# Kernel tuning notes

Measured on AMD Instinct MI355X. Metric: run time of the kernel, lower is better.

## Reference

```python
import jax, jax.numpy as jnp
import numpy as np

B, C, H, W = 4, 96, 64, 64
NLAYERS, DSTATE, EXPAND, DCONV = 2, 16, 2, 4
DIN = EXPAND * C          # 192
DTRANK = (C + 15) // 16   # 6
EPS = 1e-5


def setup_inputs() -> dict:
    key = jax.random.key(0)
    ks = jax.random.split(key, 10)
    s = jnp.float32(0.02)
    f32 = jnp.float32
    inp = {
        "x": jax.random.normal(ks[0], (B, C, H, W), f32),
        "ln_g": jnp.ones((NLAYERS, C), f32),
        "ln_b": jnp.zeros((NLAYERS, C), f32),
        "in_w": jax.random.normal(ks[1], (NLAYERS, C, 2 * DIN), f32) * s,
        "conv_w": jax.random.normal(ks[2], (NLAYERS, DIN, DCONV), f32) * s,
        "conv_b": jnp.zeros((NLAYERS, DIN), f32),
        "xproj_w": jax.random.normal(ks[3], (NLAYERS, DIN, DTRANK + 2 * DSTATE), f32) * s,
        "dt_w": jax.random.normal(ks[4], (NLAYERS, DTRANK, DIN), f32) * s,
        "dt_b": jnp.full((NLAYERS, DIN), -4.6, f32),  # softplus(-4.6) ~ 0.01
        "A_log": jnp.log(jnp.tile(jnp.arange(1, DSTATE + 1, dtype=f32)[None, None, :], (NLAYERS, DIN, 1))),
        "Dp": jnp.ones((NLAYERS, DIN), f32),
        "out_w": jax.random.normal(ks[5], (NLAYERS, DIN, C), f32) * s,
        "gp_w": jax.random.normal(ks[6], (C, C), f32) * s,
        "gp_b": jnp.zeros((C,), f32),
        "fus_w": jax.random.normal(ks[7], (C, 2 * C), f32) * s,
        "fus_b": jnp.zeros((C,), f32),
        "bn_g": jnp.ones((C,), f32),
        "bn_b": jnp.zeros((C,), f32),
    }
    return inp


def _mamba_block(seq, ln_g, ln_b, in_w, conv_w, conv_b, xproj_w, dt_w, dt_b, A_log, Dp, out_w):
    # seq: (B, L, C)
    L = seq.shape[1]
    mu = seq.mean(-1, keepdims=True)
    var = ((seq - mu) ** 2).mean(-1, keepdims=True)
    h = (seq - mu) * jax.lax.rsqrt(var + EPS) * ln_g + ln_b
    xz = h @ in_w                                   # (B, L, 2*DIN)
    xs, z = jnp.split(xz, 2, axis=-1)
    # causal depthwise conv1d along L (kernel DCONV)
    xp = jnp.pad(xs, ((0, 0), (DCONV - 1, 0), (0, 0)))
    xc = sum(conv_w[:, k] * xp[:, k:k + L, :] for k in range(DCONV)) + conv_b
    xc = jax.nn.silu(xc)
    dbl = xc @ xproj_w                              # (B, L, DTRANK+2*DSTATE)
    dt = dbl[..., :DTRANK]
    Bm = dbl[..., DTRANK:DTRANK + DSTATE]
    Cm = dbl[..., DTRANK + DSTATE:]
    delta = jax.nn.softplus(dt @ dt_w + dt_b)       # (B, L, DIN)
    A = -jnp.exp(A_log)                             # (DIN, DSTATE)
    dA = jnp.exp(delta[..., None] * A)              # (B, L, DIN, DSTATE)
    dBx = delta[..., None] * Bm[:, :, None, :] * xc[..., None]
    def comb(a, b):  # compose linear recurrences h -> A*h + u
        return (a[0] * b[0], b[0] * a[1] + b[1])
    hstates = jax.lax.associative_scan(comb, (dA, dBx), axis=1)[1]
    y = jnp.einsum('blds,bls->bld', hstates, Cm) + Dp * xc
    y = y * jax.nn.silu(z)
    return y @ out_w


def _forward(x, ln_g, ln_b, in_w, conv_w, conv_b, xproj_w, dt_w, dt_b, A_log, Dp, out_w,
             gp_w, gp_b, fus_w, fus_b, bn_g, bn_b):
    b, c, h, w = x.shape
    L = h * w
    residual = x
    seq = x.reshape(b, c, L).transpose(0, 2, 1)     # (B, L, C)
    for i in range(NLAYERS):
        seq = seq + _mamba_block(seq, ln_g[i], ln_b[i], in_w[i], conv_w[i], conv_b[i],
                                 xproj_w[i], dt_w[i], dt_b[i], A_log[i], Dp[i], out_w[i])
    mamba_out = seq.transpose(0, 2, 1).reshape(b, c, h, w)
    # global pool -> 1x1 conv -> relu -> bilinear upsample of 1x1 == broadcast
    gp = jax.nn.relu(x.mean((2, 3)) @ gp_w.T + gp_b)          # (B, C)
    gfull = jnp.broadcast_to(gp[:, :, None, None], (b, c, h, w))
    cat = jnp.concatenate([mamba_out, gfull], axis=1)         # (B, 2C, H, W)
    out = jnp.einsum('oc,bchw->bohw', fus_w, cat) + fus_b[None, :, None, None]
    # BatchNorm2d (training-mode batch statistics)
    mu = out.mean((0, 2, 3))
    var = out.var((0, 2, 3))
    out = (out - mu[None, :, None, None]) * jax.lax.rsqrt(var + EPS)[None, :, None, None]
    out = out * bn_g[None, :, None, None] + bn_b[None, :, None, None]
    return out + residual


def reference(x, ln_g, ln_b, in_w, conv_w, conv_b, xproj_w, dt_w, dt_b, A_log, Dp, out_w,
              gp_w, gp_b, fus_w, fus_b, bn_g, bn_b):
    return _forward(x, ln_g, ln_b, in_w, conv_w, conv_b, xproj_w, dt_w, dt_b, A_log, Dp, out_w,
                    gp_w, gp_b, fus_w, fus_b, bn_g, bn_b)
```

## Files before the change

### kernel.cpp

```cpp
#include <hip/hip_runtime.h>
#include <math.h>

#define BB 4
#define C 96
#define LL 4096
#define DIN 192
#define DS 16
#define DT 6
#define DX 38
#define NCHAIN (BB*DIN*DS)
#define NBLK_FUSE 512
#define EPSF 1e-5f

__device__ __forceinline__ float silu_f(float x){ return x / (1.0f + __expf(-x)); }
__device__ __forceinline__ float softplus_f(float x){ return x > 20.0f ? x : log1pf(__expf(x)); }

__global__ void k_transpose_in(const float* __restrict__ x, float* __restrict__ seq){
    __shared__ float t[32][33];
    int b = blockIdx.z;
    int l0 = blockIdx.x*32, c0 = blockIdx.y*32;
    int tx = threadIdx.x, ty = threadIdx.y;
    t[ty][tx] = x[((size_t)b*C + c0 + ty)*LL + l0 + tx];
    __syncthreads();
    seq[((size_t)b*LL + l0 + ty)*C + c0 + tx] = t[tx][ty];
}

__global__ void k_xmean(const float* __restrict__ x, float* __restrict__ xmean){
    __shared__ float red[256];
    int bc = blockIdx.x;
    const float* p = x + (size_t)bc*LL;
    float s = 0.f;
    for (int i = threadIdx.x; i < LL; i += 256) s += p[i];
    red[threadIdx.x] = s; __syncthreads();
    for (int o = 128; o; o >>= 1){
        if (threadIdx.x < o) red[threadIdx.x] += red[threadIdx.x+o];
        __syncthreads();
    }
    if (threadIdx.x == 0) xmean[bc] = red[0] * (1.f/LL);
}

__global__ void k_prep_fusw(const float* __restrict__ fus_w, float* __restrict__ fus_wt){
    int idx = blockIdx.x*256 + threadIdx.x;
    if (idx < C*C){
        int c = idx / C, o = idx % C;
        fus_wt[idx] = fus_w[(size_t)o*(2*C) + c];
    }
}

#define XSB_OFF 0
#define HB_OFF  6720
#define XCB_OFF 6720
#define DBL_OFF 0
#define FRONT_LDS 12896

__global__ __launch_bounds__(512) void k_front(const float* __restrict__ seq,
        const float* __restrict__ ln_g, const float* __restrict__ ln_b,
        const float* __restrict__ in_w,
        const float* __restrict__ conv_w, const float* __restrict__ conv_b,
        const float* __restrict__ xproj_w, const float* __restrict__ dt_w,
        const float* __restrict__ dt_b,
        float* __restrict__ zbuf, float* __restrict__ xc,
        float* __restrict__ delta, float* __restrict__ Bm, float* __restrict__ Cm){
    __shared__ float buf[FRONT_LDS];
    float* xsb = buf + XSB_OFF;
    float* hb  = buf + HB_OFF;
    float* xcb = buf + XCB_OFF;
    float* dbl = buf + DBL_OFF;
    int tid = threadIdx.x;
    int wave = tid >> 6, lane = tid & 63;
    int bid = blockIdx.x;
    int role = bid >> 9;
    int t0 = (bid & 511)*32;
    int l0 = t0 & (LL - 1);

    if (role == 1){
        for (int r = wave; r < 32; r += 8){
            const float* row = seq + (size_t)(t0 + r)*C;
            float v0 = row[lane];
            float v1 = (lane < 32) ? row[64 + lane] : 0.f;
            float sum = v0 + v1;
            for (int off = 32; off; off >>= 1) sum += __shfl_xor(sum, off);
            float mu = sum * (1.f/C);
            float d0 = v0 - mu;
            float d1 = (lane < 32) ? (v1 - mu) : 0.f;
            float sq = d0*d0 + d1*d1;
            for (int off = 32; off; off >>= 1) sq += __shfl_xor(sq, off);
            float rstd = rsqrtf(sq * (1.f/C) + EPSF);
            hb[r*C + lane] = d0*rstd*ln_g[lane] + ln_b[lane];
            if (lane < 32) hb[r*C + 64 + lane] = d1*rstd*ln_g[64+lane] + ln_b[64+lane];
        }
        __syncthreads();
        float acc[4][3];
        #pragma unroll
        for (int k = 0; k < 4; k++)
            #pragma unroll
            for (int j = 0; j < 3; j++) acc[k][j] = 0.f;
        int tw = wave*4;
        for (int c = 0; c < C; c++){
            const float* wr = in_w + (size_t)c*(2*DIN) + DIN;
            float w0 = wr[lane], w1 = wr[lane+64], w2 = wr[lane+128];
            #pragma unroll
            for (int k = 0; k < 4; k++){
                float hv = hb[(tw + k)*C + c];
                acc[k][0] = fmaf(hv, w0, acc[k][0]);
                acc[k][1] = fmaf(hv, w1, acc[k][1]);
                acc[k][2] = fmaf(hv, w2, acc[k][2]);
            }
        }
        #pragma unroll
        for (int k = 0; k < 4; k++){
            float* zp = zbuf + (size_t)(t0 + tw + k)*DIN;
            zp[lane]       = acc[k][0];
            zp[64 + lane]  = acc[k][1];
            zp[128 + lane] = acc[k][2];
        }
        return;
    }

    for (int r = wave; r < 35; r += 8){
        bool valid = (l0 > 0) || (r >= 3);
        float h0 = 0.f, h1 = 0.f;
        if (valid){
            const float* row = seq + (size_t)(t0 - 3 + r)*C;
            float v0 = row[lane];
            float v1 = (lane < 32) ? row[64 + lane] : 0.f;
            float sum = v0 + v1;
            for (int off = 32; off; off >>= 1) sum += __shfl_xor(sum, off);
            float mu = sum * (1.f/C);
            float d0 = v0 - mu;
            float d1 = (lane < 32) ? (v1 - mu) : 0.f;
            float sq = d0*d0 + d1*d1;
            for (int off = 32; off; off >>= 1) sq += __shfl_xor(sq, off);
            float rstd = rsqrtf(sq * (1.f/C) + EPSF);
            h0 = d0*rstd*ln_g[lane] + ln_b[lane];
            if (lane < 32) h1 = d1*rstd*ln_g[64+lane] + ln_b[64+lane];
        }
        hb[r*C + lane] = h0;
        if (lane < 32) hb[r*C + 64 + lane] = h1;
    }
    __syncthreads();
    int rows[5];
    #pragma unroll
    for (int k = 0; k < 5; k++){
        int r = wave + 8*k;
        rows[k] = (r < 35) ? r : 34;
    }
    float acc[5][3];
    #pragma unroll
    for (int k = 0; k < 5; k++)
        #pragma unroll
        for (int j = 0; j < 3; j++) acc[k][j] = 0.f;
    for (int c = 0; c < C; c++){
        const float* wr = in_w + (size_t)c*(2*DIN);
        float w0 = wr[lane], w1 = wr[lane+64], w2 = wr[lane+128];
        #pragma unroll
        for (int k = 0; k < 5; k++){
            float hv = hb[rows[k]*C + c];
            acc[k][0] = fmaf(hv, w0, acc[k][0]);
            acc[k][1] = fmaf(hv, w1, acc[k][1]);
            acc[k][2] = fmaf(hv, w2, acc[k][2]);
        }
    }
    #pragma unroll
    for (int k = 0; k < 5; k++){
        int r = wave + 8*k;
        if (r < 35){
            xsb[r*DIN + lane]       = acc[k][0];
            xsb[r*DIN + 64 + lane]  = acc[k][1];
            xsb[r*DIN + 128 + lane] = acc[k][2];
        }
    }
    __syncthreads();
    for (int idx = tid; idx < 32*DIN; idx += 512){
        int tl = idx / DIN, d = idx % DIN;
        const float* cw = conv_w + d*4;
        float a = conv_b[d];
        a = fmaf(cw[0], xsb[(tl+0)*DIN + d], a);
        a = fmaf(cw[1], xsb[(tl+1)*DIN + d], a);
        a = fmaf(cw[2], xsb[(tl+2)*DIN + d], a);
        a = fmaf(cw[3], xsb[(tl+3)*DIN + d], a);
        float s = silu_f(a);
        xcb[tl*(DIN+1) + d] = s;
        xc[(size_t)(t0 + tl)*DIN + d] = s;
    }
    __syncthreads();
    for (int idx = tid; idx < 32*DX; idx += 512){
        int tl = idx / DX, o = idx % DX;
        const float* wo = xproj_w + o;
        float a0 = 0.f, a1 = 0.f;
        for (int c = 0; c < DIN; c += 2){
            a0 = fmaf(xcb[tl*(DIN+1) + c],   wo[(size_t)c*DX],     a0);
            a1 = fmaf(xcb[tl*(DIN+1) + c+1], wo[(size_t)(c+1)*DX], a1);
        }
        float a = a0 + a1;
        dbl[tl*DX + o] = a;
        int tg = t0 + tl;
        if (o >= DT && o < DT+DS)      Bm[(size_t)tg*DS + (o-DT)] = a;
        else if (o >= DT+DS)           Cm[(size_t)tg*DS + (o-DT-DS)] = a;
    }
    __syncthreads();
    for (int idx = tid; idx < 32*DIN; idx += 512){
        int tl = idx / DIN, d = idx % DIN;
        float a = dt_b[d];
        #pragma unroll
        for (int r = 0; r < DT; r++) a = fmaf(dbl[tl*DX + r], dt_w[r*DIN + d], a);
        delta[(size_t)(t0 + tl)*DIN + d] = softplus_f(a);
    }
}

template<int NCHT>
__global__ __launch_bounds__(384) void k_scan_A(const float* __restrict__ delta,
        const float* __restrict__ xc, const float* __restrict__ Bm,
        const float* __restrict__ A_log,
        float* __restrict__ Pbuf, float* __restrict__ Sbuf){
    const int CLT = LL / NCHT;
    int tid = threadIdx.x;
    int d = tid >> 1, half = tid & 1;
    int ch = blockIdx.x % NCHT;
    int b  = blockIdx.x / NCHT;
    const float4* ap = (const float4*)(A_log + (size_t)d*DS + half*8);
    float4 a0 = ap[0], a1 = ap[1];
    float Av[8] = {a0.x,a0.y,a0.z,a0.w, a1.x,a1.y,a1.z,a1.w};
    float P[8], hs[8];
    #pragma unroll
    for (int s = 0; s < 8; s++){ Av[s] = -__expf(Av[s]); P[s] = 1.f; hs[s] = 0.f; }
    size_t tbase = (size_t)b*LL + (size_t)ch*CLT;
    const float*  dp = delta + tbase*DIN + d;
    const float*  xp = xc    + tbase*DIN + d;
    const float4* bp = (const float4*)(Bm + tbase*DS + half*8);
    for (int i = 0; i < CLT; i++){
        float dv = dp[(size_t)i*DIN];
        float xv = xp[(size_t)i*DIN];
        float4 b0 = bp[4*i], b1 = bp[4*i+1];
        float bb[8] = {b0.x,b0.y,b0.z,b0.w, b1.x,b1.y,b1.z,b1.w};
        float dxv = dv*xv;
        #pragma unroll
        for (int s = 0; s < 8; s++){
            float dA = __expf(dv*Av[s]);
            hs[s] = fmaf(dA, hs[s], bb[s]*dxv);
            P[s] *= dA;
        }
    }
    size_t base = (size_t)ch*NCHAIN + ((size_t)b*DIN + d)*DS + half*8;
    float4* Pb = (float4*)(Pbuf + base);
    float4* Sb = (float4*)(Sbuf + base);
    Pb[0] = make_float4(P[0],P[1],P[2],P[3]);
    Pb[1] = make_float4(P[4],P[5],P[6],P[7]);
    Sb[0] = make_float4(hs[0],hs[1],hs[2],hs[3]);
    Sb[1] = make_float4(hs[4],hs[5],hs[6],hs[7]);
}

template<int NCHT>
__global__ void k_scan_B(const float* __restrict__ Pbuf, float* __restrict__ Sbuf){
    int chain = blockIdx.x*256 + threadIdx.x;
    float h = 0.f;
    for (int ch = 0; ch < NCHT; ch++){
        size_t idx = (size_t)ch*NCHAIN + chain;
        float P = Pbuf[idx];
        float S = Sbuf[idx];
        Sbuf[idx] = h;
        h = fmaf(P, h, S);
    }
}

template<int NCHT>
__global__ __launch_bounds__(384) void k_scan_C(const float* __restrict__ delta,
        const float* __restrict__ xc, const float* __restrict__ Bm,
        const float* __restrict__ Cm,
        const float* __restrict__ A_log, const float* __restrict__ Dp,
        const float* __restrict__ Sbuf, float* __restrict__ yraw){
    const int CLT = LL / NCHT;
    int tid = threadIdx.x;
    int d = tid >> 1, half = tid & 1;
    int ch = blockIdx.x % NCHT;
    int b  = blockIdx.x / NCHT;
    const float4* ap = (const float4*)(A_log + (size_t)d*DS + half*8);
    float4 a0 = ap[0], a1 = ap[1];
    float Av[8] = {a0.x,a0.y,a0.z,a0.w, a1.x,a1.y,a1.z,a1.w};
    #pragma unroll
    for (int s = 0; s < 8; s++) Av[s] = -__expf(Av[s]);
    float Dv = Dp[d];
    size_t base = (size_t)ch*NCHAIN + ((size_t)b*DIN + d)*DS + half*8;
    const float4* Sb = (const float4*)(Sbuf + base);
    float4 h0 = Sb[0], h1 = Sb[1];
    float h[8] = {h0.x,h0.y,h0.z,h0.w, h1.x,h1.y,h1.z,h1.w};
    size_t tbase = (size_t)b*LL + (size_t)ch*CLT;
    const float*  dp = delta + tbase*DIN + d;
    const float*  xp = xc    + tbase*DIN + d;
    const float4* bp = (const float4*)(Bm + tbase*DS + half*8);
    const float4* cp = (const float4*)(Cm + tbase*DS + half*8);
    float* yp = yraw + tbase*DIN + d;
    for (int i = 0; i < CLT; i++){
        float dv = dp[(size_t)i*DIN];
        float xv = xp[(size_t)i*DIN];
        float4 b0 = bp[4*i], b1 = bp[4*i+1];
        float4 c0 = cp[4*i], c1 = cp[4*i+1];
        float bb[8] = {b0.x,b0.y,b0.z,b0.w, b1.x,b1.y,b1.z,b1.w};
        float cc[8] = {c0.x,c0.y,c0.z,c0.w, c1.x,c1.y,c1.z,c1.w};
        float dxv = dv*xv;
        float acc0 = 0.f, acc1 = 0.f;
        #pragma unroll
        for (int s = 0; s < 8; s += 2){
            float dA0 = __expf(dv*Av[s]);
            float dA1 = __expf(dv*Av[s+1]);
            h[s]   = fmaf(dA0, h[s],   bb[s]*dxv);
            h[s+1] = fmaf(dA1, h[s+1], bb[s+1]*dxv);
            acc0 = fmaf(h[s],   cc[s],   acc0);
            acc1 = fmaf(h[s+1], cc[s+1], acc1);
        }
        float contrib = acc0 + acc1;
        if (half == 0) contrib += Dv*xv;
        contrib += __shfl_xor(contrib, 1);
        if (half == 0) yp[(size_t)i*DIN] = contrib;
    }
}

__global__ __launch_bounds__(512) void k_outproj(const float* __restrict__ yraw,
        const float* __restrict__ zbuf, const float* __restrict__ out_w,
        float* __restrict__ seq){
    __shared__ float ygb[32][DIN];
    int tid = threadIdx.x;
    int wave = tid >> 6, lane = tid & 63;
    int t0 = blockIdx.x*32;
    for (int idx = tid; idx < 32*DIN; idx += 512){
        int tl = idx / DIN, d = idx % DIN;
        int t = t0 + tl;
        float yv = yraw[(size_t)t*DIN + d];
        float zv = zbuf[(size_t)t*DIN + d];
        ygb[tl][d] = yv * silu_f(zv);
    }
    __syncthreads();
    float a0[4], a1[4];
    #pragma unroll
    for (int t = 0; t < 4; t++){ a0[t] = 0.f; a1[t] = 0.f; }
    int tw = wave*4;
    for (int d = 0; d < DIN; d++){
        const float* wr = out_w + (size_t)d*C;
        float w0 = wr[lane];
        float w1 = (lane < 32) ? wr[64 + lane] : 0.f;
        #pragma unroll
        for (int t = 0; t < 4; t++){
            float yv = ygb[tw + t][d];
            a0[t] = fmaf(yv, w0, a0[t]);
            a1[t] = fmaf(yv, w1, a1[t]);
        }
    }
    #pragma unroll
    for (int t = 0; t < 4; t++){
        size_t tg = (size_t)(t0 + tw + t);
        seq[tg*C + lane] += a0[t];
        if (lane < 32) seq[tg*C + 64 + lane] += a1[t];
    }
}

__global__ void k_gp(const float* __restrict__ xmean, const float* __restrict__ gp_w,
        const float* __restrict__ gp_b, const float* __restrict__ fus_w,
        const float* __restrict__ fus_b, float* __restrict__ gconst){
    __shared__ float gp[BB*C];
    int tid = threadIdx.x;
    int b = tid / C, i = tid % C;
    float a = gp_b[i];
    for (int c = 0; c < C; c++) a = fmaf(xmean[b*C + c], gp_w[i*C + c], a);
    gp[tid] = fmaxf(a, 0.f);
    __syncthreads();
    float g = fus_b[i];
    for (int c = 0; c < C; c++) g = fmaf(fus_w[i*(2*C) + C + c], gp[b*C + c], g);
    gconst[tid] = g;
}

__global__ __launch_bounds__(512) void k_fuse(const float* __restrict__ seq,
        const float* __restrict__ fus_wt, const float* __restrict__ gconst,
        float* __restrict__ outpre, float* __restrict__ psum, float* __restrict__ psq){
    __shared__ float sb[32][C];
    __shared__ float bs[8][C], bq[8][C];
    int tid = threadIdx.x;
    int wave = tid >> 6, lane = tid & 63;
    int t0 = blockIdx.x*32;
    int b = t0 >> 12;
    for (int idx = tid; idx < 32*C; idx += 512){
        int tl = idx / C, c = idx % C;
        sb[tl][c] = seq[(size_t)(t0 + tl)*C + c];
    }
    __syncthreads();
    float g0 = gconst[b*C + lane];
    float g1 = (lane < 32) ? gconst[b*C + 64 + lane] : 0.f;
    float a0[4], a1[4];
    #pragma unroll
    for (int t = 0; t < 4; t++){ a0[t] = g0; a1[t] = g1; }
    int tw = wave*4;
    for (int c = 0; c < C; c++){
        const float* wr = fus_wt + (size_t)c*C;
        float w0 = wr[lane];
        float w1 = (lane < 32) ? wr[64 + lane] : 0.f;
        #pragma unroll
        for (int t = 0; t < 4; t++){
            float sv = sb[tw + t][c];
            a0[t] = fmaf(sv, w0, a0[t]);
            a1[t] = fmaf(sv, w1, a1[t]);
        }
    }
    float s0 = 0.f, q0 = 0.f, s1 = 0.f, q1 = 0.f;
    #pragma unroll
    for (int t = 0; t < 4; t++){
        size_t tg = (size_t)(t0 + tw + t);
        outpre[tg*C + lane] = a0[t];
        s0 += a0[t]; q0 += a0[t]*a0[t];
        if (lane < 32){
            outpre[tg*C + 64 + lane] = a1[t];
            s1 += a1[t]; q1 += a1[t]*a1[t];
        }
    }
    bs[wave][lane] = s0; bq[wave][lane] = q0;
    if (lane < 32){ bs[wave][64+lane] = s1; bq[wave][64+lane] = q1; }
    __syncthreads();
    if (tid < C){
        float s = 0.f, q = 0.f;
        #pragma unroll
        for (int w = 0; w < 8; w++){ s += bs[w][tid]; q += bq[w][tid]; }
        psum[(size_t)blockIdx.x*C + tid] = s;
        psq [(size_t)blockIdx.x*C + tid] = q;
    }
}

__global__ void k_bnstat(const float* __restrict__ psum, const float* __restrict__ psq,
        const float* __restrict__ bn_g, const float* __restrict__ bn_b,
        float* __restrict__ scale, float* __restrict__ shift){
    __shared__ float r1[256], r2[256];
    int o = blockIdx.x;
    float s1 = 0.f, s2 = 0.f;
    for (int i = threadIdx.x; i < NBLK_FUSE; i += 256){
        s1 += psum[(size_t)i*C + o];
        s2 += psq [(size_t)i*C + o];
    }
    r1[threadIdx.x] = s1; r2[threadIdx.x] = s2; __syncthreads();
    for (int off = 128; off; off >>= 1){
        if (threadIdx.x < off){ r1[threadIdx.x] += r1[threadIdx.x+off]; r2[threadIdx.x] += r2[threadIdx.x+off]; }
        __syncthreads();
    }
    if (threadIdx.x == 0){
        float N = (float)(BB*LL);
        float mu = r1[0] / N;
        float var = r2[0] / N - mu*mu;
        float sc = bn_g[o] * rsqrtf(var + EPSF);
        scale[o] = sc;
        shift[o] = bn_b[o] - mu*sc;
    }
}

__global__ void k_final(const float* __restrict__ outpre, const float* __restrict__ x,
        const float* __restrict__ scale, const float* __restrict__ shift,
        float* __restrict__ out){
    __shared__ float tle[32][33];
    int b = blockIdx.z;
    int l0 = blockIdx.x*32, o0 = blockIdx.y*32;
    int tx = threadIdx.x, ty = threadIdx.y;
    tle[ty][tx] = outpre[((size_t)b*LL + l0 + ty)*C + o0 + tx];
    __syncthreads();
    int o = o0 + ty;
    size_t idx = ((size_t)b*C + o)*LL + l0 + tx;
    out[idx] = tle[tx][ty]*scale[o] + shift[o] + x[idx];
}

extern "C" void kernel_launch(void* const* d_in, const int* in_sizes, int n_in,
                              void* d_out, int out_size, void* d_ws, size_t ws_size,
                              hipStream_t stream){
    const float* x      = (const float*)d_in[0];
    const float* ln_g   = (const float*)d_in[1];
    const float* ln_b   = (const float*)d_in[2];
    const float* in_w   = (const float*)d_in[3];
    const float* conv_w = (const float*)d_in[4];
    const float* conv_b = (const float*)d_in[5];
    const float* xproj_w= (const float*)d_in[6];
    const float* dt_w   = (const float*)d_in[7];
    const float* dt_b   = (const float*)d_in[8];
    const float* A_log  = (const float*)d_in[9];
    const float* Dp     = (const float*)d_in[10];
    const float* out_w  = (const float*)d_in[11];
    const float* gp_w   = (const float*)d_in[12];
    const float* gp_b   = (const float*)d_in[13];
    const float* fus_w  = (const float*)d_in[14];
    const float* fus_b  = (const float*)d_in[15];
    const float* bn_g   = (const float*)d_in[16];
    const float* bn_b   = (const float*)d_in[17];

    const size_t base_f = (size_t)BB*LL*C
                        + (size_t)BB*LL*DIN
                        + (size_t)BB*LL*DIN
                        + (size_t)BB*LL*DIN
                        + (size_t)BB*LL*DS + (size_t)BB*LL*DS;
    const size_t small_f = BB*C + BB*C + C + C + (size_t)C*C;
    const size_t need256 = (base_f + 2*(size_t)256*NCHAIN + small_f) * sizeof(float);
    const int nch = (ws_size >= need256) ? 256 : 128;

    float* ws    = (float*)d_ws;
    float* seq   = ws;
    float* zbuf  = seq   + (size_t)BB*LL*C;
    float* xcbuf = zbuf  + (size_t)BB*LL*DIN;
    float* delta = xcbuf + (size_t)BB*LL*DIN;
    float* Bmb   = delta + (size_t)BB*LL*DIN;
    float* Cmb   = Bmb   + (size_t)BB*LL*DS;
    float* Pbuf  = Cmb   + (size_t)BB*LL*DS;
    float* Sbuf  = Pbuf  + (size_t)nch*NCHAIN;
    float* xmean = Sbuf  + (size_t)nch*NCHAIN;
    float* gconst= xmean + BB*C;
    float* scale = gconst+ BB*C;
    float* shift = scale + C;
    float* fus_wt= shift + C;
    float* yraw  = delta;
    float* outpre= zbuf;
    float* psum  = zbuf + (size_t)BB*LL*C;
    float* psq   = psum + (size_t)NBLK_FUSE*C;

    k_transpose_in<<<dim3(LL/32, C/32, BB), dim3(32,32), 0, stream>>>(x, seq);
    k_xmean<<<BB*C, 256, 0, stream>>>(x, xmean);
    k_prep_fusw<<<(C*C + 255)/256, 256, 0, stream>>>(fus_w, fus_wt);

    for (int layer = 0; layer < 2; layer++){
        const float* lng = ln_g   + (size_t)layer*C;
        const float* lnb = ln_b   + (size_t)layer*C;
        const float* inw = in_w   + (size_t)layer*C*2*DIN;
        const float* cw  = conv_w + (size_t)layer*DIN*4;
        const float* cb  = conv_b + (size_t)layer*DIN;
        const float* xpw = xproj_w+ (size_t)layer*DIN*DX;
        const float* dtw = dt_w   + (size_t)layer*DT*DIN;
        const float* dtb = dt_b   + (size_t)layer*DIN;
        const float* alog= A_log  + (size_t)layer*DIN*DS;
        const float* dpp = Dp     + (size_t)layer*DIN;
        const float* ow  = out_w  + (size_t)layer*DIN*C;

        k_front<<<2*(BB*LL)/32, 512, 0, stream>>>(seq, lng, lnb, inw, cw, cb,
                                                  xpw, dtw, dtb, zbuf, xcbuf, delta, Bmb, Cmb);
        if (nch == 256){
            k_scan_A<256><<<BB*256, 384, 0, stream>>>(delta, xcbuf, Bmb, alog, Pbuf, Sbuf);
            k_scan_B<256><<<NCHAIN/256, 256, 0, stream>>>(Pbuf, Sbuf);
            k_scan_C<256><<<BB*256, 384, 0, stream>>>(delta, xcbuf, Bmb, Cmb, alog, dpp, Sbuf, yraw);
        } else {
            k_scan_A<128><<<BB*128, 384, 0, stream>>>(delta, xcbuf, Bmb, alog, Pbuf, Sbuf);
            k_scan_B<128><<<NCHAIN/256, 256, 0, stream>>>(Pbuf, Sbuf);
            k_scan_C<128><<<BB*128, 384, 0, stream>>>(delta, xcbuf, Bmb, Cmb, alog, dpp, Sbuf, yraw);
        }
        k_outproj<<<(BB*LL)/32, 512, 0, stream>>>(yraw, zbuf, ow, seq);
    }

    k_gp<<<1, BB*C, 0, stream>>>(xmean, gp_w, gp_b, fus_w, fus_b, gconst);
    k_fuse<<<(BB*LL)/32, 512, 0, stream>>>(seq, fus_wt, gconst, outpre, psum, psq);
    k_bnstat<<<C, 256, 0, stream>>>(psum, psq, bn_g, bn_b, scale, shift);
    k_final<<<dim3(LL/32, C/32, BB), dim3(32,32), 0, stream>>>(outpre, x, scale, shift, (float*)d_out);
}
```

Baseline: 382.1 us.

## Recompute z-gate projection inside out-projection kernel instead of storing zbuf

Removes the z-branch role from the front kernel and drops the zbuf workspace. The out-projection kernel now recomputes LayerNorm of seq and the z half of in_proj, then applies the silu gate before out_proj. This saves a full (B,L,DIN) write and read to global memory per layer, and halves the front kernel grid. The cost is extra per-block arithmetic and weight loads in k_outproj, plus a longer critical path in that kernel.

```diff
diff --git a/kernel.cpp b/kernel.cpp
--- a/kernel.cpp
+++ b/kernel.cpp
@@ -59,7 +59,7 @@
         const float* __restrict__ conv_w, const float* __restrict__ conv_b,
         const float* __restrict__ xproj_w, const float* __restrict__ dt_w,
         const float* __restrict__ dt_b,
-        float* __restrict__ zbuf, float* __restrict__ xc,
+        float* __restrict__ xc,
         float* __restrict__ delta, float* __restrict__ Bm, float* __restrict__ Cm){
     __shared__ float buf[FRONT_LDS];
     float* xsb = buf + XSB_OFF;
@@ -68,55 +68,8 @@
     float* dbl = buf + DBL_OFF;
     int tid = threadIdx.x;
     int wave = tid >> 6, lane = tid & 63;
-    int bid = blockIdx.x;
-    int role = bid >> 9;
-    int t0 = (bid & 511)*32;
+    int t0 = blockIdx.x*32;
     int l0 = t0 & (LL - 1);
-
-    if (role == 1){
-        for (int r = wave; r < 32; r += 8){
-            const float* row = seq + (size_t)(t0 + r)*C;
-            float v0 = row[lane];
-            float v1 = (lane < 32) ? row[64 + lane] : 0.f;
-            float sum = v0 + v1;
-            for (int off = 32; off; off >>= 1) sum += __shfl_xor(sum, off);
-            float mu = sum * (1.f/C);
-            float d0 = v0 - mu;
-            float d1 = (lane < 32) ? (v1 - mu) : 0.f;
-            float sq = d0*d0 + d1*d1;
-            for (int off = 32; off; off >>= 1) sq += __shfl_xor(sq, off);
-            float rstd = rsqrtf(sq * (1.f/C) + EPSF);
-            hb[r*C + lane] = d0*rstd*ln_g[lane] + ln_b[lane];
-            if (lane < 32) hb[r*C + 64 + lane] = d1*rstd*ln_g[64+lane] + ln_b[64+lane];
-        }
-        __syncthreads();
-        float acc[4][3];
-        #pragma unroll
-        for (int k = 0; k < 4; k++)
-            #pragma unroll
-            for (int j = 0; j < 3; j++) acc[k][j] = 0.f;
-        int tw = wave*4;
-        for (int c = 0; c < C; c++){
-            const float* wr = in_w + (size_t)c*(2*DIN) + DIN;
-            float w0 = wr[lane], w1 = wr[lane+64], w2 = wr[lane+128];
-            #pragma unroll
-            for (int k = 0; k < 4; k++){
-                float hv = hb[(tw + k)*C + c];
-                acc[k][0] = fmaf(hv, w0, acc[k][0]);
-                acc[k][1] = fmaf(hv, w1, acc[k][1]);
-                acc[k][2] = fmaf(hv, w2, acc[k][2]);
-            }
-        }
-        #pragma unroll
-        for (int k = 0; k < 4; k++){
-            float* zp = zbuf + (size_t)(t0 + tw + k)*DIN;
-            zp[lane]       = acc[k][0];
-            zp[64 + lane]  = acc[k][1];
-            zp[128 + lane] = acc[k][2];
-        }
-        return;
-    }
-
     for (int r = wave; r < 35; r += 8){
         bool valid = (l0 > 0) || (r >= 3);
         float h0 = 0.f, h1 = 0.f;
@@ -316,38 +269,79 @@
 }
 
 __global__ __launch_bounds__(512) void k_outproj(const float* __restrict__ yraw,
-        const float* __restrict__ zbuf, const float* __restrict__ out_w,
+        const float* __restrict__ ln_g, const float* __restrict__ ln_b,
+        const float* __restrict__ in_w, const float* __restrict__ out_w,
         float* __restrict__ seq){
+    __shared__ float hb[32][C];
     __shared__ float ygb[32][DIN];
     int tid = threadIdx.x;
     int wave = tid >> 6, lane = tid & 63;
     int t0 = blockIdx.x*32;
-    for (int idx = tid; idx < 32*DIN; idx += 512){
-        int tl = idx / DIN, d = idx % DIN;
-        int t = t0 + tl;
-        float yv = yraw[(size_t)t*DIN + d];
-        float zv = zbuf[(size_t)t*DIN + d];
-        ygb[tl][d] = yv * silu_f(zv);
+    int tw4 = wave*4;
+    #pragma unroll
+    for (int tt = 0; tt < 4; tt++){
+        int tl = tw4 + tt;
+        const float* row = seq + (size_t)(t0 + tl)*C;
+        float v0 = row[lane];
+        float v1 = (lane < 32) ? row[64 + lane] : 0.f;
+        float sum = v0 + v1;
+        for (int off = 32; off; off >>= 1) sum += __shfl_xor(sum, off);
+        float mu = sum * (1.f/C);
+        float d0 = v0 - mu;
+        float d1 = (lane < 32) ? (v1 - mu) : 0.f;
+        float sq = d0*d0 + d1*d1;
+        for (int off = 32; off; off >>= 1) sq += __shfl_xor(sq, off);
+        float rstd = rsqrtf(sq * (1.f/C) + EPSF);
+        hb[tl][lane] = d0*rstd*ln_g[lane] + ln_b[lane];
+        if (lane < 32) hb[tl][64+lane] = d1*rstd*ln_g[64+lane] + ln_b[64+lane];
+    }
+    __syncthreads();
+    {
+        float zacc[4][3];
+        #pragma unroll
+        for (int k = 0; k < 4; k++)
+            #pragma unroll
+            for (int j = 0; j < 3; j++) zacc[k][j] = 0.f;
+        for (int c = 0; c < C; c++){
+            const float* wr = in_w + (size_t)c*(2*DIN) + DIN;
+            float w0 = wr[lane], w1 = wr[lane+64], w2 = wr[lane+128];
+            #pragma unroll
+            for (int k = 0; k < 4; k++){
+                float hv = hb[tw4 + k][c];
+                zacc[k][0] = fmaf(hv, w0, zacc[k][0]);
+                zacc[k][1] = fmaf(hv, w1, zacc[k][1]);
+                zacc[k][2] = fmaf(hv, w2, zacc[k][2]);
+            }
+        }
+        #pragma unroll
+        for (int k = 0; k < 4; k++){
+            size_t tg = (size_t)(t0 + tw4 + k);
+            float y0 = yraw[tg*DIN + lane];
+            float y1 = yraw[tg*DIN + 64 + lane];
+            float y2 = yraw[tg*DIN + 128 + lane];
+            ygb[tw4 + k][lane]       = y0 * silu_f(zacc[k][0]);
+            ygb[tw4 + k][64 + lane]  = y1 * silu_f(zacc[k][1]);
+            ygb[tw4 + k][128 + lane] = y2 * silu_f(zacc[k][2]);
+        }
     }
     __syncthreads();
     float a0[4], a1[4];
     #pragma unroll
     for (int t = 0; t < 4; t++){ a0[t] = 0.f; a1[t] = 0.f; }
-    int tw = wave*4;
     for (int d = 0; d < DIN; d++){
         const float* wr = out_w + (size_t)d*C;
         float w0 = wr[lane];
         float w1 = (lane < 32) ? wr[64 + lane] : 0.f;
         #pragma unroll
         for (int t = 0; t < 4; t++){
-            float yv = ygb[tw + t][d];
+            float yv = ygb[tw4 + t][d];
             a0[t] = fmaf(yv, w0, a0[t]);
             a1[t] = fmaf(yv, w1, a1[t]);
         }
     }
     #pragma unroll
     for (int t = 0; t < 4; t++){
-        size_t tg = (size_t)(t0 + tw + t);
+        size_t tg = (size_t)(t0 + tw4 + t);
         seq[tg*C + lane] += a0[t];
         if (lane < 32) seq[tg*C + 64 + lane] += a1[t];
     }
@@ -486,7 +480,6 @@
     const size_t base_f = (size_t)BB*LL*C
                         + (size_t)BB*LL*DIN
                         + (size_t)BB*LL*DIN
-                        + (size_t)BB*LL*DIN
                         + (size_t)BB*LL*DS + (size_t)BB*LL*DS;
     const size_t small_f = BB*C + BB*C + C + C + (size_t)C*C;
     const size_t need256 = (base_f + 2*(size_t)256*NCHAIN + small_f) * sizeof(float);
@@ -494,8 +487,7 @@
 
     float* ws    = (float*)d_ws;
     float* seq   = ws;
-    float* zbuf  = seq   + (size_t)BB*LL*C;
-    float* xcbuf = zbuf  + (size_t)BB*LL*DIN;
+    float* xcbuf = seq   + (size_t)BB*LL*C;
     float* delta = xcbuf + (size_t)BB*LL*DIN;
     float* Bmb   = delta + (size_t)BB*LL*DIN;
     float* Cmb   = Bmb   + (size_t)BB*LL*DS;
@@ -507,8 +499,8 @@
     float* shift = scale + C;
     float* fus_wt= shift + C;
     float* yraw  = delta;
-    float* outpre= zbuf;
-    float* psum  = zbuf + (size_t)BB*LL*C;
+    float* outpre= xcbuf;
+    float* psum  = xcbuf + (size_t)BB*LL*C;
     float* psq   = psum + (size_t)NBLK_FUSE*C;
 
     k_transpose_in<<<dim3(LL/32, C/32, BB), dim3(32,32), 0, stream>>>(x, seq);
@@ -528,8 +520,8 @@
         const float* dpp = Dp     + (size_t)layer*DIN;
         const float* ow  = out_w  + (size_t)layer*DIN*C;
 
-        k_front<<<2*(BB*LL)/32, 512, 0, stream>>>(seq, lng, lnb, inw, cw, cb,
-                                                  xpw, dtw, dtb, zbuf, xcbuf, delta, Bmb, Cmb);
+        k_front<<<(BB*LL)/32, 512, 0, stream>>>(seq, lng, lnb, inw, cw, cb,
+                                                xpw, dtw, dtb, xcbuf, delta, Bmb, Cmb);
         if (nch == 256){
             k_scan_A<256><<<BB*256, 384, 0, stream>>>(delta, xcbuf, Bmb, alog, Pbuf, Sbuf);
             k_scan_B<256><<<NCHAIN/256, 256, 0, stream>>>(Pbuf, Sbuf);
@@ -539,7 +531,7 @@
             k_scan_B<128><<<NCHAIN/256, 256, 0, stream>>>(Pbuf, Sbuf);
             k_scan_C<128><<<BB*128, 384, 0, stream>>>(delta, xcbuf, Bmb, Cmb, alog, dpp, Sbuf, yraw);
         }
-        k_outproj<<<(BB*LL)/32, 512, 0, stream>>>(yraw, zbuf, ow, seq);
+        k_outproj<<<(BB*LL)/32, 512, 0, stream>>>(yraw, lng, lnb, inw, ow, seq);
     }
 
     k_gp<<<1, BB*C, 0, stream>>>(xmean, gp_w, gp_b, fus_w, fus_b, gconst);
```

Result: faster. 336.8 us (-11.8%).
